# Kernel tuning notes

Measured on AMD Instinct MI355X. Metric: run time of the kernel, lower is better.

The kernel has to match this reference:

```python
import jax, jax.numpy as jnp
import numpy as np


def setup_inputs() -> dict:
    key = jax.random.key(0)
    k1, k2, k3 = jax.random.split(key, 3)
    B, C, H, W = 16, 64, 256, 256
    x = jax.random.normal(k1, (B, C, H, W), dtype=jnp.float32)
    g = jax.random.normal(k2, (B, C, H, W), dtype=jnp.float32)
    gamma = jax.random.normal(k3, (1,), dtype=jnp.float32)
    return {"x": x, "g": g, "gamma": gamma}


def reference(x, g, gamma):
    # x, g: (B, C, H, W); gamma: (1,)
    B, C, H, W = x.shape
    N = H * W
    xq = x.reshape(B, C, N)   # proj_query / proj_value
    gq = g.reshape(B, C, N)

    # channel-channel energy from x: (B, C, C)
    energy = jnp.einsum('bcn,bdn->bcd', xq, xq)
    attention = jax.nn.softmax(energy, axis=-1)

    # channel-channel energy from guide g: (B, C, C)
    energy_guide = jnp.einsum('bcn,bdn->bcd', gq, gq)
    attention_guide = jax.nn.softmax(energy_guide, axis=-1)

    # chained attention: (B, C, C)
    guide_energy = jnp.einsum('bcd,bde->bce', attention, attention_guide)
    guide_energy_new = jnp.max(guide_energy, axis=-1, keepdims=True) - guide_energy
    guide_attention = jax.nn.softmax(guide_energy_new, axis=-1)

    # apply to values and residual
    out = jnp.einsum('bcd,bdn->bcn', guide_attention, xq).reshape(B, C, H, W)
    return gamma[0] * out + x
```

## Files before the change

kernel.cpp:

```cpp
#include <hip/hip_runtime.h>


typedef _Float16 h8 __attribute__((ext_vector_type(8)));
typedef float    f4 __attribute__((ext_vector_type(4)));
typedef __fp16   p2 __attribute__((ext_vector_type(2)));
typedef unsigned long long ull;

#define NB 16
#define NC 64
#define NPIX 65536
#define GRAM_CHUNK 1024
#define PASS_PX 128
#define NPASS (GRAM_CHUNK / PASS_PX)
#define NCHUNK (NPIX / GRAM_CHUNK)
#define ROW_H 136
#define LDS_H (64 * ROW_H + 64)

#define AP_NPX 256
#define XT_ROW 72

__device__ __forceinline__ int rowbase_h(int c) {
    return c * ROW_H + (c >> 3) * 8;
}

__device__ __forceinline__ unsigned int pk(float a, float b) {
    p2 v = __builtin_amdgcn_cvt_pkrtz(a, b);
    return __builtin_bit_cast(unsigned int, v);
}

__global__ __launch_bounds__(512, 2) void gram_kernel(
    const float* __restrict__ x, const float* __restrict__ g,
    float* __restrict__ part)
{
    __shared__ __align__(16) _Float16 lds[2][2 * LDS_H];

    const int tid = threadIdx.x;
    const int b = blockIdx.y;
    const size_t cbase = (size_t)b * NC * NPIX + (size_t)blockIdx.x * GRAM_CHUNK;

    const int w     = tid >> 6;
    const int lane  = tid & 63;
    const int mtx   = w >> 2;
    const int rb    = w & 3;
    const int l15   = lane & 15;
    const int khalf = lane >> 4;
    const int abase_h = rowbase_h(rb * 16 + l15);

    const int sc = tid >> 5;
    const int sq = tid & 31;
    const size_t soff = (size_t)sc * NPIX + sq * 4;
    const int lds_off = rowbase_h(sc) + sq * 4;

    f4 acc[4];
    #pragma unroll
    for (int cb = 0; cb < 4; ++cb) acc[cb] = (f4){0.f, 0.f, 0.f, 0.f};

    f4 rx[4], rg[4];
    #pragma unroll
    for (int it = 0; it < 4; ++it) {
        rx[it] = *(const f4*)(x + cbase + soff + (size_t)it * 16 * NPIX);
        rg[it] = *(const f4*)(g + cbase + soff + (size_t)it * 16 * NPIX);
    }

    for (int pass = 0; pass < NPASS; ++pass) {
        _Float16* xs = lds[pass & 1];
        _Float16* gs = lds[pass & 1] + LDS_H;

        #pragma unroll
        for (int it = 0; it < 4; ++it) {
            ull hx = (ull)pk(rx[it].x, rx[it].y) | ((ull)pk(rx[it].z, rx[it].w) << 32);
            ull hg = (ull)pk(rg[it].x, rg[it].y) | ((ull)pk(rg[it].z, rg[it].w) << 32);
            int off = lds_off + it * 16 * ROW_H + it * 2 * 8;
            *reinterpret_cast<ull*>(&xs[off]) = hx;
            *reinterpret_cast<ull*>(&gs[off]) = hg;
        }

        if (pass + 1 < NPASS) {
            const size_t pbase = cbase + (size_t)(pass + 1) * PASS_PX;
            #pragma unroll
            for (int it = 0; it < 4; ++it) {
                rx[it] = *(const f4*)(x + pbase + soff + (size_t)it * 16 * NPIX);
                rg[it] = *(const f4*)(g + pbase + soff + (size_t)it * 16 * NPIX);
            }
        }

        __syncthreads();

        const _Float16* mybuf = mtx ? gs : xs;
        #pragma unroll
        for (int ks = 0; ks < 4; ++ks) {
            int koff = ks * 32 + khalf * 8;
            h8 a = *reinterpret_cast<const h8*>(&mybuf[abase_h + koff]);
            #pragma unroll
            for (int cb = 0; cb < 4; ++cb) {
                h8 bf = *reinterpret_cast<const h8*>(&mybuf[rowbase_h(cb * 16 + l15) + koff]);
                acc[cb] = __builtin_amdgcn_mfma_f32_16x16x32_f16(a, bf, acc[cb], 0, 0, 0);
            }
        }
    }

    float* po = part + (((size_t)blockIdx.x * NB + b) * 2 + mtx) * 4096;
    #pragma unroll
    for (int cb = 0; cb < 4; ++cb)
        #pragma unroll
        for (int r = 0; r < 4; ++r)
            po[(rb * 16 + khalf * 4 + r) * 64 + cb * 16 + l15] = acc[cb][r];
}

__global__ __launch_bounds__(256) void reduce_kernel(
    const float* __restrict__ part, float* __restrict__ ex, float* __restrict__ eg)
{
    const int idx = blockIdx.x * 256 + threadIdx.x;
    const int bm = idx >> 12;
    const int cd = idx & 4095;
    float s = 0.f;
    #pragma unroll 8
    for (int ch = 0; ch < NCHUNK; ++ch)
        s += part[(size_t)ch * (NB * 2 * 4096) + (size_t)bm * 4096 + cd];
    float* dst = (bm & 1) ? eg : ex;
    dst[(bm >> 1) * 4096 + cd] = s;
}

__global__ __launch_bounds__(256) void chain_kernel(
    const float* __restrict__ ex, const float* __restrict__ eg,
    const float* __restrict__ gammap, float* __restrict__ M)
{
    __shared__ float A1[64][68];
    __shared__ float A2[64][68];
    __shared__ float red[64][4];

    const int b = blockIdx.x;
    const int tid = threadIdx.x;

    if (tid < 64) {
        const int c = tid;
        float r[64];
        #pragma unroll
        for (int d = 0; d < 64; ++d) r[d] = ex[b * 4096 + c * 64 + d];
        float mx = r[0];
        #pragma unroll
        for (int d = 1; d < 64; ++d) mx = fmaxf(mx, r[d]);
        float s = 0.f;
        #pragma unroll
        for (int d = 0; d < 64; ++d) { r[d] = expf(r[d] - mx); s += r[d]; }
        float inv = 1.f / s;
        #pragma unroll
        for (int d = 0; d < 64; ++d) A1[c][d] = r[d] * inv;

        #pragma unroll
        for (int d = 0; d < 64; ++d) r[d] = eg[b * 4096 + c * 64 + d];
        mx = r[0];
        #pragma unroll
        for (int d = 1; d < 64; ++d) mx = fmaxf(mx, r[d]);
        s = 0.f;
        #pragma unroll
        for (int d = 0; d < 64; ++d) { r[d] = expf(r[d] - mx); s += r[d]; }
        inv = 1.f / s;
        #pragma unroll
        for (int d = 0; d < 64; ++d) A2[c][d] = r[d] * inv;
    }
    __syncthreads();

    const int c = tid >> 2, sq = tid & 3;
    float ge[16];
    #pragma unroll
    for (int k = 0; k < 16; ++k) ge[k] = 0.f;
    for (int d = 0; d < 64; ++d) {
        float a = A1[c][d];
        const float* row = &A2[d][sq * 16];
        #pragma unroll
        for (int k = 0; k < 16; ++k) ge[k] = fmaf(a, row[k], ge[k]);
    }

    float mx = ge[0];
    #pragma unroll
    for (int k = 1; k < 16; ++k) mx = fmaxf(mx, ge[k]);
    red[c][sq] = mx;
    __syncthreads();
    float gm = fmaxf(fmaxf(red[c][0], red[c][1]), fmaxf(red[c][2], red[c][3]));
    __syncthreads();

    float gen[16];
    #pragma unroll
    for (int k = 0; k < 16; ++k) gen[k] = gm - ge[k];
    float mx2 = gen[0];
    #pragma unroll
    for (int k = 1; k < 16; ++k) mx2 = fmaxf(mx2, gen[k]);
    red[c][sq] = mx2;
    __syncthreads();
    float m2 = fmaxf(fmaxf(red[c][0], red[c][1]), fmaxf(red[c][2], red[c][3]));
    __syncthreads();

    float p[16];
    float s = 0.f;
    #pragma unroll
    for (int k = 0; k < 16; ++k) { p[k] = expf(gen[k] - m2); s += p[k]; }
    red[c][sq] = s;
    __syncthreads();
    float S = red[c][0] + red[c][1] + red[c][2] + red[c][3];

    float gam = gammap[0];
    float invS = 1.f / S;
    #pragma unroll
    for (int k = 0; k < 16; ++k) {
        int e = sq * 16 + k;
        M[b * 4096 + c * 64 + e] = gam * p[k] * invS;
    }
}

__global__ __launch_bounds__(256) void apply_kernel(
    const float* __restrict__ x, const float* __restrict__ M,
    float* __restrict__ out)
{
    __shared__ __align__(16) _Float16 xT[AP_NPX * XT_ROW];
    __shared__ __align__(16) _Float16 Ml[64 * XT_ROW];

    const int tid = threadIdx.x;
    const int b = blockIdx.y;
    const int n0 = blockIdx.x * AP_NPX;
    const float* xb = x + (size_t)b * NC * NPIX + n0;

    #pragma unroll
    for (int it = 0; it < 8; ++it) {
        int e = it * 256 + tid;
        int q  = e & 63;
        int dp = e >> 6;
        f4 va = *(const f4*)(xb + (size_t)(2 * dp)     * NPIX + q * 4);
        f4 vb = *(const f4*)(xb + (size_t)(2 * dp + 1) * NPIX + q * 4);
        #pragma unroll
        for (int j = 0; j < 4; ++j) {
            float aj = (j == 0) ? va.x : (j == 1) ? va.y : (j == 2) ? va.z : va.w;
            float bj = (j == 0) ? vb.x : (j == 1) ? vb.y : (j == 2) ? vb.z : vb.w;
            *reinterpret_cast<unsigned int*>(&xT[(q * 4 + j) * XT_ROW + 2 * dp]) = pk(aj, bj);
        }
    }
    const float* Mb = M + b * 4096;
    #pragma unroll
    for (int it = 0; it < 4; ++it) {
        int e = it * 256 + tid;
        int c  = e >> 4;
        int qq = e & 15;
        f4 mv = *(const f4*)(Mb + c * 64 + qq * 4);
        *reinterpret_cast<unsigned int*>(&Ml[c * XT_ROW + qq * 4])     = pk(mv.x, mv.y);
        *reinterpret_cast<unsigned int*>(&Ml[c * XT_ROW + qq * 4 + 2]) = pk(mv.z, mv.w);
    }
    __syncthreads();

    const int w    = tid >> 6;
    const int lane = tid & 63;
    const int l15  = lane & 15;
    const int kh   = lane >> 4;

    h8 bfrag[4][2];
    #pragma unroll
    for (int nb = 0; nb < 4; ++nb)
        #pragma unroll
        for (int ks = 0; ks < 2; ++ks)
            bfrag[nb][ks] = *reinterpret_cast<const h8*>(
                &xT[(w * 64 + nb * 16 + l15) * XT_ROW + ks * 32 + kh * 8]);

    f4 acc[4][4];
    #pragma unroll
    for (int cb = 0; cb < 4; ++cb)
        #pragma unroll
        for (int nb = 0; nb < 4; ++nb) acc[cb][nb] = (f4){0.f, 0.f, 0.f, 0.f};

    #pragma unroll
    for (int cb = 0; cb < 4; ++cb) {
        #pragma unroll
        for (int ks = 0; ks < 2; ++ks) {
            h8 a = *reinterpret_cast<const h8*>(
                &Ml[(cb * 16 + l15) * XT_ROW + ks * 32 + kh * 8]);
            #pragma unroll
            for (int nb = 0; nb < 4; ++nb)
                acc[cb][nb] = __builtin_amdgcn_mfma_f32_16x16x32_f16(a, bfrag[nb][ks], acc[cb][nb], 0, 0, 0);
        }
    }

    const size_t base = (size_t)b * NC * NPIX + n0 + w * 64;
    #pragma unroll
    for (int cb = 0; cb < 4; ++cb) {
        #pragma unroll
        for (int r = 0; r < 4; ++r) {
            const int row = cb * 16 + kh * 4 + r;
            #pragma unroll
            for (int nb = 0; nb < 4; ++nb) {
                size_t idx = base + (size_t)row * NPIX + nb * 16 + l15;
                out[idx] = acc[cb][nb][r] + x[idx];
            }
        }
    }
}

extern "C" void kernel_launch(void* const* d_in, const int* in_sizes, int n_in,
                              void* d_out, int out_size, void* d_ws, size_t ws_size,
                              hipStream_t stream) {
    const float* x     = (const float*)d_in[0];
    const float* g     = (const float*)d_in[1];
    const float* gamma = (const float*)d_in[2];
    float* out = (float*)d_out;
    float* ws  = (float*)d_ws;

    float* ex = ws;
    float* eg = ws + NB * 4096;
    float* M  = ws + 2 * NB * 4096;

    float* part = out;

    gram_kernel<<<dim3(NCHUNK, NB), 512, 0, stream>>>(x, g, part);
    reduce_kernel<<<512, 256, 0, stream>>>(part, ex, eg);
    chain_kernel<<<NB, 256, 0, stream>>>(ex, eg, gamma, M);
    apply_kernel<<<dim3(NPIX / AP_NPX, NB), 256, 0, stream>>>(x, M, out);
}
```

Measured before the change: 268.7 us.

## Deepen gram kernel global-load prefetch to two passes ahead with manual barriers

The gram kernel now holds two register sets of staged x/g tiles, so global loads run two passes ahead instead of one. The pass loop is unrolled by two with fixed LDS buffers. __syncthreads is replaced by an LDS-only waitcnt, a raw s_barrier and a sched_barrier, so outstanding global loads are not drained at each barrier. The aim is to hide global memory latency better, at the cost of more VGPRs and possible lower occupancy; LDS reuse safety now depends on the double-buffer timing.

```diff
diff --git a/kernel.cpp b/kernel.cpp
--- a/kernel.cpp
+++ b/kernel.cpp
@@ -51,50 +51,93 @@
     const size_t soff = (size_t)sc * NPIX + sq * 4;
     const int lds_off = rowbase_h(sc) + sq * 4;
 
+    const float* xp = x + cbase + soff;
+    const float* gp = g + cbase + soff;
+
     f4 acc[4];
     #pragma unroll
     for (int cb = 0; cb < 4; ++cb) acc[cb] = (f4){0.f, 0.f, 0.f, 0.f};
 
-    f4 rx[4], rg[4];
+    f4 rxa[4], rga[4], rxb[4], rgb[4];
     #pragma unroll
     for (int it = 0; it < 4; ++it) {
-        rx[it] = *(const f4*)(x + cbase + soff + (size_t)it * 16 * NPIX);
-        rg[it] = *(const f4*)(g + cbase + soff + (size_t)it * 16 * NPIX);
-    }
-
-    for (int pass = 0; pass < NPASS; ++pass) {
-        _Float16* xs = lds[pass & 1];
-        _Float16* gs = lds[pass & 1] + LDS_H;
-
-        #pragma unroll
-        for (int it = 0; it < 4; ++it) {
-            ull hx = (ull)pk(rx[it].x, rx[it].y) | ((ull)pk(rx[it].z, rx[it].w) << 32);
-            ull hg = (ull)pk(rg[it].x, rg[it].y) | ((ull)pk(rg[it].z, rg[it].w) << 32);
-            int off = lds_off + it * 16 * ROW_H + it * 2 * 8;
-            *reinterpret_cast<ull*>(&xs[off]) = hx;
-            *reinterpret_cast<ull*>(&gs[off]) = hg;
-        }
-
-        if (pass + 1 < NPASS) {
-            const size_t pbase = cbase + (size_t)(pass + 1) * PASS_PX;
+        rxa[it] = *(const f4*)(xp + (size_t)it * 16 * NPIX);
+        rga[it] = *(const f4*)(gp + (size_t)it * 16 * NPIX);
+    }
+    #pragma unroll
+    for (int it = 0; it < 4; ++it) {
+        rxb[it] = *(const f4*)(xp + PASS_PX + (size_t)it * 16 * NPIX);
+        rgb[it] = *(const f4*)(gp + PASS_PX + (size_t)it * 16 * NPIX);
+    }
+
+    #pragma unroll
+    for (int kk = 0; kk < NPASS; kk += 2) {
+        {
+            _Float16* xs = lds[0];
+            _Float16* gs = lds[0] + LDS_H;
             #pragma unroll
             for (int it = 0; it < 4; ++it) {
-                rx[it] = *(const f4*)(x + pbase + soff + (size_t)it * 16 * NPIX);
-                rg[it] = *(const f4*)(g + pbase + soff + (size_t)it * 16 * NPIX);
-            }
-        }
-
-        __syncthreads();
-
-        const _Float16* mybuf = mtx ? gs : xs;
-        #pragma unroll
-        for (int ks = 0; ks < 4; ++ks) {
-            int koff = ks * 32 + khalf * 8;
-            h8 a = *reinterpret_cast<const h8*>(&mybuf[abase_h + koff]);
-            #pragma unroll
-            for (int cb = 0; cb < 4; ++cb) {
-                h8 bf = *reinterpret_cast<const h8*>(&mybuf[rowbase_h(cb * 16 + l15) + koff]);
-                acc[cb] = __builtin_amdgcn_mfma_f32_16x16x32_f16(a, bf, acc[cb], 0, 0, 0);
+                ull hx = (ull)pk(rxa[it].x, rxa[it].y) | ((ull)pk(rxa[it].z, rxa[it].w) << 32);
+                ull hg = (ull)pk(rga[it].x, rga[it].y) | ((ull)pk(rga[it].z, rga[it].w) << 32);
+                int off = lds_off + it * 16 * ROW_H + it * 2 * 8;
+                *reinterpret_cast<ull*>(&xs[off]) = hx;
+                *reinterpret_cast<ull*>(&gs[off]) = hg;
+            }
+            if (kk + 2 < NPASS) {
+                const size_t pb = (size_t)(kk + 2) * PASS_PX;
+                #pragma unroll
+                for (int it = 0; it < 4; ++it) {
+                    rxa[it] = *(const f4*)(xp + pb + (size_t)it * 16 * NPIX);
+                    rga[it] = *(const f4*)(gp + pb + (size_t)it * 16 * NPIX);
+                }
+            }
+            asm volatile("s_waitcnt lgkmcnt(0)" ::: "memory");
+            __builtin_amdgcn_s_barrier();
+            __builtin_amdgcn_sched_barrier(0);
+            const _Float16* mybuf = mtx ? gs : xs;
+            #pragma unroll
+            for (int ks = 0; ks < 4; ++ks) {
+                int koff = ks * 32 + khalf * 8;
+                h8 a = *reinterpret_cast<const h8*>(&mybuf[abase_h + koff]);
+                #pragma unroll
+                for (int cb = 0; cb < 4; ++cb) {
+                    h8 bf = *reinterpret_cast<const h8*>(&mybuf[rowbase_h(cb * 16 + l15) + koff]);
+                    acc[cb] = __builtin_amdgcn_mfma_f32_16x16x32_f16(a, bf, acc[cb], 0, 0, 0);
+                }
+            }
+        }
+        {
+            _Float16* xs = lds[1];
+            _Float16* gs = lds[1] + LDS_H;
+            #pragma unroll
+            for (int it = 0; it < 4; ++it) {
+                ull hx = (ull)pk(rxb[it].x, rxb[it].y) | ((ull)pk(rxb[it].z, rxb[it].w) << 32);
+                ull hg = (ull)pk(rgb[it].x, rgb[it].y) | ((ull)pk(rgb[it].z, rgb[it].w) << 32);
+                int off = lds_off + it * 16 * ROW_H + it * 2 * 8;
+                *reinterpret_cast<ull*>(&xs[off]) = hx;
+                *reinterpret_cast<ull*>(&gs[off]) = hg;
+            }
+            if (kk + 3 < NPASS) {
+                const size_t pb = (size_t)(kk + 3) * PASS_PX;
+                #pragma unroll
+                for (int it = 0; it < 4; ++it) {
+                    rxb[it] = *(const f4*)(xp + pb + (size_t)it * 16 * NPIX);
+                    rgb[it] = *(const f4*)(gp + pb + (size_t)it * 16 * NPIX);
+                }
+            }
+            asm volatile("s_waitcnt lgkmcnt(0)" ::: "memory");
+            __builtin_amdgcn_s_barrier();
+            __builtin_amdgcn_sched_barrier(0);
+            const _Float16* mybuf = mtx ? gs : xs;
+            #pragma unroll
+            for (int ks = 0; ks < 4; ++ks) {
+                int koff = ks * 32 + khalf * 8;
+                h8 a = *reinterpret_cast<const h8*>(&mybuf[abase_h + koff]);
+                #pragma unroll
+                for (int cb = 0; cb < 4; ++cb) {
+                    h8 bf = *reinterpret_cast<const h8*>(&mybuf[rowbase_h(cb * 16 + l15) + koff]);
+                    acc[cb] = __builtin_amdgcn_mfma_f32_16x16x32_f16(a, bf, acc[cb], 0, 0, 0);
+                }
             }
         }
     }
```

Result: slower. 279.6 us (+4.0%).
